# Optimization experiments

Hardware: AMD Instinct MI355X
Metric: run time of the kernel (lower is better)

## Reference

```python
import jax, jax.numpy as jnp
import numpy as np

B, S, HID = 1, 2048, 4096
H, KV, D, R = 32, 8, 128, 64   # heads, kv heads, head_dim, rotary_dim
EPS = 1e-6
THETA = 10000.0


def setup_inputs() -> dict:
    key = jax.random.key(0)
    ks = jax.random.split(key, 6)
    sc = 0.02
    return {
        'hidden_states': jax.random.normal(ks[0], (B, S, HID), jnp.float32),
        'Wq': jax.random.normal(ks[1], (H * D, HID), jnp.float32) * sc,
        'Wk': jax.random.normal(ks[2], (KV * D, HID), jnp.float32) * sc,
        'Wv': jax.random.normal(ks[3], (KV * D, HID), jnp.float32) * sc,
        'Wo': jax.random.normal(ks[4], (HID, H * D), jnp.float32) * sc,
        'q_norm_w': jnp.ones((H * D,), jnp.float32),
        'k_norm_w': jnp.ones((KV * D,), jnp.float32),
        'position_ids': jnp.broadcast_to(jnp.arange(S, dtype=jnp.int64)[None, :], (B, S)),
    }


def _rms_norm(x, w):
    xf = x.astype(jnp.float32)
    var = jnp.mean(xf * xf, axis=-1, keepdims=True)
    return (w * (xf * jax.lax.rsqrt(var + EPS))).astype(x.dtype)


def _rotate_half(x):
    x1, x2 = x[..., : R // 2], x[..., R // 2:]
    return jnp.concatenate((-x2, x1), axis=-1)


def reference(hidden_states, Wq, Wk, Wv, Wo, q_norm_w, k_norm_w, position_ids):
    x = hidden_states
    # projections (torch Linear: y = x @ W^T)
    q = jnp.einsum('bsd,od->bso', x, Wq)                      # [B,S,H*D]
    k = jnp.einsum('bsd,od->bso', x, Wk)                      # [B,S,KV*D]
    v = jnp.einsum('bsd,od->bso', x, Wv).reshape(B, S, KV, D)
    # QK RMSNorm over flattened head dims
    q = _rms_norm(q, q_norm_w).reshape(B, S, H, D)
    k = _rms_norm(k, k_norm_w).reshape(B, S, KV, D)
    # partial RoPE: rotary_dim=R out of head_dim=D
    inv_freq = 1.0 / (THETA ** (jnp.arange(0, R, 2, dtype=jnp.float32) / R))  # [R/2]
    freqs = position_ids.astype(jnp.float32)[..., None] * inv_freq            # [B,S,R/2]
    emb = jnp.concatenate((freqs, freqs), axis=-1)                            # [B,S,R]
    cos = jnp.cos(emb)[:, :, None, :]                                         # [B,S,1,R]
    sin = jnp.sin(emb)[:, :, None, :]
    q_rot = q[..., :R] * cos + _rotate_half(q[..., :R]) * sin
    k_rot = k[..., :R] * cos + _rotate_half(k[..., :R]) * sin
    q = jnp.concatenate((q_rot, q[..., R:]), axis=-1)
    k = jnp.concatenate((k_rot, k[..., R:]), axis=-1)
    # GQA repeat_kv
    G = H // KV
    k = jnp.repeat(k, G, axis=2)  # [B,S,H,D]
    v = jnp.repeat(v, G, axis=2)
    # attention with causal mask, softmax in fp32
    scaling = D ** -0.5
    scores = jnp.einsum('bqhd,bkhd->bhqk', q, k) * scaling    # [B,H,S,S]
    causal = jnp.tril(jnp.ones((S, S), dtype=bool))
    scores = jnp.where(causal[None, None], scores, jnp.finfo(jnp.float32).min)
    attn = jax.nn.softmax(scores.astype(jnp.float32), axis=-1).astype(q.dtype)
    out = jnp.einsum('bhqk,bkhd->bqhd', attn, v).reshape(B, S, H * D)
    return jnp.einsum('bso,do->bsd', out, Wo)
```

## Files before the change

kernel.cpp:

```cpp
#include <hip/hip_runtime.h>
#include <hip/hip_bf16.h>
#include <math.h>

typedef __bf16 bf16;
typedef __bf16 bf16x8 __attribute__((ext_vector_type(8)));
typedef float f32x4 __attribute__((ext_vector_type(4)));

#define S_LEN 2048
#define HID_D 4096
#define NH 32
#define NKV 8
#define HD 128
#define SCALE_LOG2 (0.08838834764831843f * 1.4426950408889634f)
#define FIXED_M 17.0f

__device__ __forceinline__ void gload_lds16(const void* g, void* lds) {
  __builtin_amdgcn_global_load_lds((__attribute__((address_space(1))) void*)g,
                                   (__attribute__((address_space(3))) void*)lds, 16, 0, 0);
}

#define MEMFENCE asm volatile("" ::: "memory")

__device__ __forceinline__ void cvt_range(const float* __restrict__ in,
                                          bf16* __restrict__ out, int n8,
                                          int start, int stride) {
  for (int i = start; i < n8; i += stride) {
    const float4* p = (const float4*)in + 2 * (size_t)i;
    float4 a = p[0], b = p[1];
    bf16x8 o;
    o[0] = (bf16)a.x; o[1] = (bf16)a.y; o[2] = (bf16)a.z; o[3] = (bf16)a.w;
    o[4] = (bf16)b.x; o[5] = (bf16)b.y; o[6] = (bf16)b.z; o[7] = (bf16)b.w;
    *((bf16x8*)out + i) = o;
  }
}

__global__ __launch_bounds__(256) void cvt4_kernel(const float* __restrict__ s0,
                                                   const float* __restrict__ s1,
                                                   const float* __restrict__ s2,
                                                   const float* __restrict__ s3,
                                                   bf16* __restrict__ d0,
                                                   bf16* __restrict__ d1,
                                                   bf16* __restrict__ d2,
                                                   bf16* __restrict__ d3,
                                                   int n0, int n1, int n2, int n3) {
  int start = blockIdx.x * blockDim.x + threadIdx.x;
  int stride = gridDim.x * blockDim.x;
  cvt_range(s0, d0, n0, start, stride);
  cvt_range(s1, d1, n1, start, stride);
  cvt_range(s2, d2, n2, start, stride);
  cvt_range(s3, d3, n3, start, stride);
}

__global__ __launch_bounds__(256) void cvt_kernel(const float* __restrict__ in,
                                                  bf16* __restrict__ out, int n8) {
  int i = blockIdx.x * blockDim.x + threadIdx.x;
  int stride = gridDim.x * blockDim.x;
  cvt_range(in, out, n8, i, stride);
}

template <int BM, int BN>
__global__ __launch_bounds__(512, 2) void gemm_s(const bf16* __restrict__ A,
                                                 const bf16* __restrict__ B,
                                                 float* __restrict__ C,
                                                 int N, int Kfull, int T) {
  constexpr int MFr = BM / 32;
  constexpr int NFr = BN / 64;
  constexpr int NL = (BM + BN) / 64;
  constexpr int TILE = (BM + BN) * 128;

  __shared__ __align__(16) char lds[2 * TILE];
  const int t = threadIdx.x, l = t & 63, w = t >> 6;
  const int wr = w >> 2, wc = w & 3;
  const int l15 = l & 15, lg = l >> 4;

  const int GX = gridDim.x, GY = gridDim.y;
  const int lin = blockIdx.y * GX + blockIdx.x;
  const int x = lin & 7, j = lin >> 3;
  const int rectW = GX >> 2, rectH = GY >> 1;
  const int rx = x & 3, ry = x >> 2;
  const int jn = j % rectW, jm = j / rectW;
  const int n0 = (rx * rectW + jn) * BN;
  const int m0 = (ry * rectH + jm) * BM;

  auto stage = [&](int d, int tau) {
    char* dst = lds + d * TILE;
    const size_t kpos = (size_t)tau * 64;
#pragma unroll
    for (int i = 0; i < NL; i++) {
      int q = i * 512 + t;
      int r = q >> 3;
      int c = (q & 7) ^ (r & 7);
      const bf16* src = (i * 512 < BM * 8)
                            ? (A + (size_t)(m0 + r) * Kfull)
                            : (B + (size_t)(n0 + (r - BM)) * Kfull);
      gload_lds16(src + kpos + c * 8, dst + q * 16);
    }
  };

  f32x4 acc[MFr][NFr] = {};

  stage(0, 0);
  asm volatile("s_waitcnt vmcnt(0)" ::: "memory");
  MEMFENCE; __builtin_amdgcn_s_barrier(); MEMFENCE;

  for (int tau = 0; tau < T; tau++) {
    const int d = tau & 1;
    if (tau + 1 < T) stage(d ^ 1, tau + 1);

    const char* Ab = lds + d * TILE;
    const char* Bb = Ab + BM * 128;
    bf16x8 a[MFr][2], b[NFr][2];
#pragma unroll
    for (int mf = 0; mf < MFr; mf++) {
      const int row = wr * (BM / 2) + mf * 16 + l15;
#pragma unroll
      for (int ks = 0; ks < 2; ks++)
        a[mf][ks] = *(const bf16x8*)(Ab + row * 128 + (((ks * 4 + lg) ^ (row & 7)) << 4));
    }
#pragma unroll
    for (int nf = 0; nf < NFr; nf++) {
      const int row = wc * (BN / 4) + nf * 16 + l15;
#pragma unroll
      for (int ks = 0; ks < 2; ks++)
        b[nf][ks] = *(const bf16x8*)(Bb + row * 128 + (((ks * 4 + lg) ^ (row & 7)) << 4));
    }
#pragma unroll
    for (int mf = 0; mf < MFr; mf++)
#pragma unroll
      for (int nf = 0; nf < NFr; nf++)
#pragma unroll
        for (int ks = 0; ks < 2; ks++)
          acc[mf][nf] = __builtin_amdgcn_mfma_f32_16x16x32_bf16(a[mf][ks], b[nf][ks],
                                                               acc[mf][nf], 0, 0, 0);

    asm volatile("s_waitcnt vmcnt(0)" ::: "memory");
    MEMFENCE; __builtin_amdgcn_s_barrier(); MEMFENCE;
  }

#pragma unroll
  for (int mf = 0; mf < MFr; mf++) {
    int row = m0 + wr * (BM / 2) + mf * 16 + lg * 4;
#pragma unroll
    for (int nf = 0; nf < NFr; nf++) {
      int col = n0 + wc * (BN / 4) + nf * 16 + l15;
      float* Cp = C + (size_t)row * N + col;
#pragma unroll
      for (int rr = 0; rr < 4; rr++) Cp[(size_t)rr * N] = acc[mf][nf][rr];
    }
  }
}

__global__ __launch_bounds__(256) void vt_kernel(const float* __restrict__ QKV,
                                                 bf16* __restrict__ Vt) {
  __shared__ __align__(16) float tile[64][68];
  const int s0 = blockIdx.x * 64, d0 = blockIdx.y * 64;
  const int t = threadIdx.x;
#pragma unroll
  for (int i = 0; i < 4; i++) {
    int row = i * 16 + (t >> 4);
    int c4 = t & 15;
    float4 v = *(const float4*)(QKV + (size_t)(s0 + row) * 6144 + 5120 + d0 + c4 * 4);
    *(float4*)&tile[row][c4 * 4] = v;
  }
  __syncthreads();
#pragma unroll
  for (int i = 0; i < 2; i++) {
    int slot = i * 256 + t;
    int dr = slot >> 3, ch = slot & 7;
    bf16x8 o;
#pragma unroll
    for (int j = 0; j < 8; j++) o[j] = (bf16)tile[ch * 8 + j][dr];
    *(bf16x8*)(Vt + (size_t)(d0 + dr) * S_LEN + s0 + ch * 8) = o;
  }
}

__global__ __launch_bounds__(256) void prep_kernel(const float* __restrict__ QKV,
                                                   const float* __restrict__ qw,
                                                   const float* __restrict__ kw,
                                                   const int* __restrict__ pos_ids,
                                                   bf16* __restrict__ Qb,
                                                   bf16* __restrict__ Kb) {
  __shared__ __align__(16) float row[5120];
  __shared__ float cs[64];
  __shared__ float red[8];
  const int s = blockIdx.x, t = threadIdx.x;

  const float4* src = (const float4*)(QKV + (size_t)s * 6144);
#pragma unroll
  for (int i = 0; i < 5; i++) ((float4*)row)[t + i * 256] = src[t + i * 256];

  if (t < 32) {
    float p = (float)pos_ids[s];
    float ang = p * powf(10000.0f, -(float)t * (1.0f / 32.0f));
    float sn, cn;
    sincosf(ang, &sn, &cn);
    cs[t] = cn;
    cs[32 + t] = sn;
  }
  __syncthreads();

  float aq = 0.f, ak = 0.f;
  for (int i = t; i < 4096; i += 256) { float v = row[i]; aq += v * v; }
  for (int i = 4096 + t; i < 5120; i += 256) { float v = row[i]; ak += v * v; }
#pragma unroll
  for (int off = 32; off; off >>= 1) {
    aq += __shfl_down(aq, off);
    ak += __shfl_down(ak, off);
  }
  if ((t & 63) == 0) { red[t >> 6] = aq; red[4 + (t >> 6)] = ak; }
  __syncthreads();
  const float scq = rsqrtf((red[0] + red[1] + red[2] + red[3]) * (1.0f / 4096.0f) + 1e-6f);
  const float sck = rsqrtf((red[4] + red[5] + red[6] + red[7]) * (1.0f / 1024.0f) + 1e-6f);

  for (int e = t; e < 4096; e += 256) {
    int d = e & 127;
    int hh = e >> 7;
    float val = row[e] * scq * qw[e];
    float o;
    if (d < 32)       o = val * cs[d] - (row[e + 32] * scq * qw[e + 32]) * cs[32 + d];
    else if (d < 64)  o = val * cs[d - 32] + (row[e - 32] * scq * qw[e - 32]) * cs[d];
    else              o = val;
    Qb[((size_t)hh * S_LEN + s) * HD + d] = (bf16)o;
  }
  for (int e = t; e < 1024; e += 256) {
    int d = e & 127;
    int hh = e >> 7;
    int ri = 4096 + e;
    float val = row[ri] * sck * kw[e];
    float o;
    if (d < 32)       o = val * cs[d] - (row[ri + 32] * sck * kw[e + 32]) * cs[32 + d];
    else if (d < 64)  o = val * cs[d - 32] + (row[ri - 32] * sck * kw[e - 32]) * cs[d];
    else              o = val;
    Kb[((size_t)hh * S_LEN + s) * HD + d] = (bf16)o;
  }
}

__global__ __launch_bounds__(256, 2) void attn_kernel(const bf16* __restrict__ Qb,
                                                      const bf16* __restrict__ Kb,
                                                      const bf16* __restrict__ Vt,
                                                      bf16* __restrict__ Ctx) {
  __shared__ __align__(16) char KB[2][16384];
  __shared__ __align__(16) char VB[2][16384];
  __shared__ __align__(16) char PB[8192];
  const int t = threadIdx.x, l = t & 63, w = t >> 6;
  const int l15 = l & 15, lg = l >> 4;
  const int pairc = blockIdx.x >> 5;
  const int h = blockIdx.x & 31;

  const bf16* Kh = Kb + (size_t)(h >> 2) * S_LEN * HD;
  const bf16* Vh = Vt + (size_t)(h >> 2) * HD * S_LEN;
  char* Pw = PB + w * 2048;

  const int kj0 = t & 15;
  const int vj0 = t & 7;

  auto stageK = [&](int buf, int kvbase) {
#pragma unroll
    for (int i = 0; i < 4; i++) {
      int r = (i * 256 + t) >> 4;
      const bf16* src = Kh + (size_t)(kvbase + r) * HD + ((kj0 ^ (r & 7)) << 3);
      gload_lds16(src, KB[buf] + (i * 256 + w * 64) * 16);
    }
  };
  auto stageV = [&](int buf, int kvbase) {
#pragma unroll
    for (int i = 0; i < 4; i++) {
      int r = (i * 256 + t) >> 3;
      const bf16* src = Vh + (size_t)r * S_LEN + kvbase + ((vj0 ^ (r & 7)) << 3);
      gload_lds16(src, VB[buf] + (i * 256 + w * 64) * 16);
    }
  };

#pragma unroll
  for (int phase = 0; phase < 2; phase++) {
    const int chunk = (phase == 0) ? pairc : (31 - pairc);
    const int ktiles = chunk + 1;
    const int q0 = chunk * 64 + w * 16;

    const bf16* Qh = Qb + ((size_t)h * S_LEN + q0) * HD;
    bf16x8 qf[4];
#pragma unroll
    for (int kk = 0; kk < 4; kk++)
      qf[kk] = *(const bf16x8*)(Qh + (size_t)l15 * HD + kk * 32 + lg * 8);

    stageK(0, 0);
    stageV(0, 0);

    f32x4 O[8] = {};
    float lsum[4] = {0.f, 0.f, 0.f, 0.f};

    for (int tt = 0; tt < ktiles; tt++) {
      const int cur = tt & 1;
      const int kv0 = tt * 64;
      const char* Kcur = KB[cur];
      const bool hasnext = (tt + 1 < ktiles);

      asm volatile("s_waitcnt vmcnt(0)" ::: "memory");
      MEMFENCE;
      __builtin_amdgcn_s_barrier();
      MEMFENCE;

      if (hasnext) {
        stageK(cur ^ 1, kv0 + 64);
        stageV(cur ^ 1, kv0 + 64);
      }

      f32x4 sc[4];
#pragma unroll
      for (int g = 0; g < 4; g++) sc[g] = (f32x4){0.f, 0.f, 0.f, 0.f};
#pragma unroll
      for (int g = 0; g < 4; g++) {
        const int r = g * 16 + l15;
        const char* Krow = Kcur + r * 256;
        const int sw = (r & 7);
#pragma unroll
        for (int kk = 0; kk < 4; kk++) {
          bf16x8 kf = *(const bf16x8*)(Krow + (((kk * 4 + lg) ^ sw) << 4));
          sc[g] = __builtin_amdgcn_mfma_f32_16x16x32_bf16(qf[kk], kf, sc[g], 0, 0, 0);
        }
      }

      const bool needmask = (kv0 + 63 > q0);
      float sv[4][4];
#pragma unroll
      for (int g = 0; g < 4; g++)
#pragma unroll
        for (int r = 0; r < 4; r++) {
          float x = fmaf(sc[g][r], SCALE_LOG2, -FIXED_M);
          if (needmask) {
            int kv = kv0 + g * 16 + l15;
            int qr = q0 + lg * 4 + r;
            if (kv > qr) x = -1e30f;
          }
          sv[g][r] = exp2f(x);
        }
#pragma unroll
      for (int r = 0; r < 4; r++)
        lsum[r] += (sv[0][r] + sv[1][r]) + (sv[2][r] + sv[3][r]);

#pragma unroll
      for (int g = 0; g < 4; g++)
#pragma unroll
        for (int r = 0; r < 4; r++) {
          int prow = lg * 4 + r;
          int csw = (prow & 3) ^ (((prow >> 2) & 3) << 1);
          int pbyte = prow * 128 + (((g * 16 + l15) * 2) ^ (csw << 4));
          *(bf16*)(Pw + pbyte) = (bf16)sv[g][r];
        }
      asm volatile("s_waitcnt lgkmcnt(0)" ::: "memory");
      const int rcsw = (l15 & 3) ^ (((l15 >> 2) & 3) << 1);
      bf16x8 pa[2];
#pragma unroll
      for (int ks = 0; ks < 2; ks++)
        pa[ks] = *(const bf16x8*)(Pw + l15 * 128 + (((ks * 4 + lg) ^ rcsw) << 4));

#pragma unroll
      for (int ks = 0; ks < 2; ks++)
#pragma unroll
        for (int dt = 0; dt < 8; dt++) {
          const int r = dt * 16 + l15;
          bf16x8 vf = *(const bf16x8*)(VB[cur] + r * 128 + (((ks * 4 + lg) ^ (r & 7)) << 4));
          O[dt] = __builtin_amdgcn_mfma_f32_16x16x32_bf16(pa[ks], vf, O[dt], 0, 0, 0);
        }
    }

    MEMFENCE;
    __builtin_amdgcn_s_barrier();
    MEMFENCE;

#pragma unroll
    for (int r = 0; r < 4; r++) {
      float x = lsum[r];
      x += __shfl_xor(x, 1);
      x += __shfl_xor(x, 2);
      x += __shfl_xor(x, 4);
      x += __shfl_xor(x, 8);
      float inv = 1.0f / x;
      bf16* Cp = Ctx + (size_t)(q0 + lg * 4 + r) * HID_D + h * HD + l15;
#pragma unroll
      for (int dt = 0; dt < 8; dt++) Cp[dt * 16] = (bf16)(O[dt][r] * inv);
    }
  }
}

extern "C" void kernel_launch(void* const* d_in, const int* in_sizes, int n_in,
                              void* d_out, int out_size, void* d_ws, size_t ws_size,
                              hipStream_t stream) {
  const float* X  = (const float*)d_in[0];
  const float* Wq = (const float*)d_in[1];
  const float* Wk = (const float*)d_in[2];
  const float* Wv = (const float*)d_in[3];
  const float* Wo = (const float*)d_in[4];
  const float* qw = (const float*)d_in[5];
  const float* kw = (const float*)d_in[6];
  const int* pos  = (const int*)d_in[7];

  char* ws = (char*)d_ws;
  bf16* Xb    = (bf16*)ws;
  bf16* Wqkvb = (bf16*)(ws + (16ll << 20));
  bf16* Wob   = Wqkvb;
  float* QKV  = (float*)(ws + (64ll << 20));
  bf16* Ctx   = (bf16*)(ws + (96ll << 20));
  bf16* Qb    = (bf16*)(ws + (112ll << 20));
  bf16* Kb    = (bf16*)(ws + (128ll << 20));
  bf16* Vt    = (bf16*)(ws + (132ll << 20));

  cvt4_kernel<<<2048, 256, 0, stream>>>(X, Wq, Wk, Wv,
                                        Xb, Wqkvb, Wqkvb + 4096 * 4096,
                                        Wqkvb + 5120 * 4096,
                                        S_LEN * HID_D / 8, 4096 * 4096 / 8,
                                        1024 * 4096 / 8, 1024 * 4096 / 8);

  gemm_s<128, 384><<<dim3(16, 16), 512, 0, stream>>>(Xb, Wqkvb, QKV, 6144, HID_D, 64);

  cvt_kernel<<<2048, 256, 0, stream>>>(Wo, Wob, 4096 * 4096 / 8);

  vt_kernel<<<dim3(32, 16), 256, 0, stream>>>(QKV, Vt);
  prep_kernel<<<S_LEN, 256, 0, stream>>>(QKV, qw, kw, pos, Qb, Kb);

  attn_kernel<<<dim3(512), 256, 0, stream>>>(Qb, Kb, Vt, Ctx);

  gemm_s<128, 256><<<dim3(16, 16), 512, 0, stream>>>(Ctx, Wob, (float*)d_out,
                                                     HID_D, HID_D, 64);
}
```

Baseline: 318.6 us.

## Deepen GEMM pipeline to four 32-wide K stages and delay attention prefetch

The GEMM is restructured from a double-buffered loop with 64-wide K steps into a four-buffer loop with 32-wide K steps. It keeps three loads in flight, waits on partial vmcnt counts instead of draining them, and uses a swizzle adjusted to the 64-byte rows. The goal is to hide global-load latency behind the MFMAs. The cost is twice as many barriers per K, fewer MFMAs per barrier, and hand-set vmcnt counts that depend on NL. In the attention kernel, the next K/V tile prefetch now issues after the QK^T MFMAs, which shifts when memory traffic overlaps compute.

```diff
diff --git a/kernel.cpp b/kernel.cpp
--- a/kernel.cpp
+++ b/kernel.cpp
@@ -59,16 +59,16 @@
 }
 
 template <int BM, int BN>
-__global__ __launch_bounds__(512, 2) void gemm_s(const bf16* __restrict__ A,
+__global__ __launch_bounds__(512, 2) void gemm_p(const bf16* __restrict__ A,
                                                  const bf16* __restrict__ B,
                                                  float* __restrict__ C,
                                                  int N, int Kfull, int T) {
   constexpr int MFr = BM / 32;
   constexpr int NFr = BN / 64;
-  constexpr int NL = (BM + BN) / 64;
-  constexpr int TILE = (BM + BN) * 128;
-
-  __shared__ __align__(16) char lds[2 * TILE];
+  constexpr int NL = (BM + BN) / 128;
+  constexpr int TILE = (BM + BN) * 64;
+
+  __shared__ __align__(16) char lds[4 * TILE];
   const int t = threadIdx.x, l = t & 63, w = t >> 6;
   const int wr = w >> 2, wc = w & 3;
   const int l15 = l & 15, lg = l >> 4;
@@ -82,58 +82,61 @@
   const int n0 = (rx * rectW + jn) * BN;
   const int m0 = (ry * rectH + jm) * BM;
 
-  auto stage = [&](int d, int tau) {
-    char* dst = lds + d * TILE;
-    const size_t kpos = (size_t)tau * 64;
+  auto stage = [&](int buf, int tau) {
+    char* dst = lds + buf * TILE;
+    const size_t kpos = (size_t)tau * 32;
 #pragma unroll
     for (int i = 0; i < NL; i++) {
       int q = i * 512 + t;
-      int r = q >> 3;
-      int c = (q & 7) ^ (r & 7);
-      const bf16* src = (i * 512 < BM * 8)
-                            ? (A + (size_t)(m0 + r) * Kfull)
-                            : (B + (size_t)(n0 + (r - BM)) * Kfull);
+      int r = q >> 2;
+      int c = (q & 3) ^ ((r >> 1) & 3);
+      const bf16* src = (r < BM) ? (A + (size_t)(m0 + r) * Kfull)
+                                 : (B + (size_t)(n0 + (r - BM)) * Kfull);
       gload_lds16(src + kpos + c * 8, dst + q * 16);
     }
   };
 
   f32x4 acc[MFr][NFr] = {};
 
-  stage(0, 0);
-  asm volatile("s_waitcnt vmcnt(0)" ::: "memory");
+  stage(0, 0); stage(1, 1); stage(2, 2);
+  if (NL == 4) { asm volatile("s_waitcnt vmcnt(8)" ::: "memory"); }
+  else         { asm volatile("s_waitcnt vmcnt(6)" ::: "memory"); }
   MEMFENCE; __builtin_amdgcn_s_barrier(); MEMFENCE;
 
   for (int tau = 0; tau < T; tau++) {
-    const int d = tau & 1;
-    if (tau + 1 < T) stage(d ^ 1, tau + 1);
+    const int d = tau & 3;
+    if (tau + 3 < T) stage((tau + 3) & 3, tau + 3);
 
     const char* Ab = lds + d * TILE;
-    const char* Bb = Ab + BM * 128;
-    bf16x8 a[MFr][2], b[NFr][2];
+    const char* Bb = Ab + BM * 64;
+    bf16x8 a[MFr], b[NFr];
 #pragma unroll
     for (int mf = 0; mf < MFr; mf++) {
       const int row = wr * (BM / 2) + mf * 16 + l15;
-#pragma unroll
-      for (int ks = 0; ks < 2; ks++)
-        a[mf][ks] = *(const bf16x8*)(Ab + row * 128 + (((ks * 4 + lg) ^ (row & 7)) << 4));
+      a[mf] = *(const bf16x8*)(Ab + row * 64 + ((lg ^ ((row >> 1) & 3)) << 4));
     }
 #pragma unroll
     for (int nf = 0; nf < NFr; nf++) {
       const int row = wc * (BN / 4) + nf * 16 + l15;
-#pragma unroll
-      for (int ks = 0; ks < 2; ks++)
-        b[nf][ks] = *(const bf16x8*)(Bb + row * 128 + (((ks * 4 + lg) ^ (row & 7)) << 4));
+      b[nf] = *(const bf16x8*)(Bb + row * 64 + ((lg ^ ((row >> 1) & 3)) << 4));
     }
 #pragma unroll
     for (int mf = 0; mf < MFr; mf++)
 #pragma unroll
       for (int nf = 0; nf < NFr; nf++)
-#pragma unroll
-        for (int ks = 0; ks < 2; ks++)
-          acc[mf][nf] = __builtin_amdgcn_mfma_f32_16x16x32_bf16(a[mf][ks], b[nf][ks],
-                                                               acc[mf][nf], 0, 0, 0);
-
-    asm volatile("s_waitcnt vmcnt(0)" ::: "memory");
+        acc[mf][nf] = __builtin_amdgcn_mfma_f32_16x16x32_bf16(a[mf], b[nf],
+                                                             acc[mf][nf], 0, 0, 0);
+
+    const int k = T - 2 - tau;
+    if (NL == 4) {
+      if (k >= 2)      { asm volatile("s_waitcnt vmcnt(8)" ::: "memory"); }
+      else if (k == 1) { asm volatile("s_waitcnt vmcnt(4)" ::: "memory"); }
+      else             { asm volatile("s_waitcnt vmcnt(0)" ::: "memory"); }
+    } else {
+      if (k >= 2)      { asm volatile("s_waitcnt vmcnt(6)" ::: "memory"); }
+      else if (k == 1) { asm volatile("s_waitcnt vmcnt(3)" ::: "memory"); }
+      else             { asm volatile("s_waitcnt vmcnt(0)" ::: "memory"); }
+    }
     MEMFENCE; __builtin_amdgcn_s_barrier(); MEMFENCE;
   }
 
@@ -300,11 +303,6 @@
       __builtin_amdgcn_s_barrier();
       MEMFENCE;
 
-      if (hasnext) {
-        stageK(cur ^ 1, kv0 + 64);
-        stageV(cur ^ 1, kv0 + 64);
-      }
-
       f32x4 sc[4];
 #pragma unroll
       for (int g = 0; g < 4; g++) sc[g] = (f32x4){0.f, 0.f, 0.f, 0.f};
@@ -318,6 +316,11 @@
           bf16x8 kf = *(const bf16x8*)(Krow + (((kk * 4 + lg) ^ sw) << 4));
           sc[g] = __builtin_amdgcn_mfma_f32_16x16x32_bf16(qf[kk], kf, sc[g], 0, 0, 0);
         }
+      }
+
+      if (hasnext) {
+        stageK(cur ^ 1, kv0 + 64);
+        stageV(cur ^ 1, kv0 + 64);
       }
 
       const bool needmask = (kv0 + 63 > q0);
@@ -411,7 +414,7 @@
                                         S_LEN * HID_D / 8, 4096 * 4096 / 8,
                                         1024 * 4096 / 8, 1024 * 4096 / 8);
 
-  gemm_s<128, 384><<<dim3(16, 16), 512, 0, stream>>>(Xb, Wqkvb, QKV, 6144, HID_D, 64);
+  gemm_p<128, 384><<<dim3(16, 16), 512, 0, stream>>>(Xb, Wqkvb, QKV, 6144, HID_D, 128);
 
   cvt_kernel<<<2048, 256, 0, stream>>>(Wo, Wob, 4096 * 4096 / 8);
 
@@ -420,6 +423,6 @@
 
   attn_kernel<<<dim3(512), 256, 0, stream>>>(Qb, Kb, Vt, Ctx);
 
-  gemm_s<128, 256><<<dim3(16, 16), 512, 0, stream>>>(Ctx, Wob, (float*)d_out,
-                                                     HID_D, HID_D, 64);
-}
+  gemm_p<128, 256><<<dim3(16, 16), 512, 0, stream>>>(Ctx, Wob, (float*)d_out,
+                                                     HID_D, HID_D, 128);
+}
```

After: 333.5 us. +4.7%, slower.

## Split-K output projection with larger tiles and move attention KV prefetch after QK

Applied to the files above, without the earlier changes.

Replaces the output-projection GEMM with a split-K variant that uses 256x256 tiles over two K halves. The halves are written to the output and to a workspace partial buffer, then summed by a separate add kernel. This keeps the grid at 256 blocks while raising per-block data reuse, at the cost of an extra 32MB read-modify-write pass and a slightly different accumulation order. Separately, the attention kernel now issues the next K/V tile loads after the QK MFMAs rather than before them, which changes how those loads overlap with compute.

```diff
diff --git a/kernel.cpp b/kernel.cpp
--- a/kernel.cpp
+++ b/kernel.cpp
@@ -58,6 +58,18 @@
   cvt_range(in, out, n8, i, stride);
 }
 
+__global__ __launch_bounds__(256) void add_kernel(float* __restrict__ out,
+                                                  const float* __restrict__ part, int n4) {
+  int i = blockIdx.x * blockDim.x + threadIdx.x;
+  int stride = gridDim.x * blockDim.x;
+  for (; i < n4; i += stride) {
+    float4 a = ((const float4*)out)[i];
+    float4 b = ((const float4*)part)[i];
+    a.x += b.x; a.y += b.y; a.z += b.z; a.w += b.w;
+    ((float4*)out)[i] = a;
+  }
+}
+
 template <int BM, int BN>
 __global__ __launch_bounds__(512, 2) void gemm_s(const bf16* __restrict__ A,
                                                  const bf16* __restrict__ B,
@@ -132,6 +144,98 @@
         for (int ks = 0; ks < 2; ks++)
           acc[mf][nf] = __builtin_amdgcn_mfma_f32_16x16x32_bf16(a[mf][ks], b[nf][ks],
                                                                acc[mf][nf], 0, 0, 0);
+
+    asm volatile("s_waitcnt vmcnt(0)" ::: "memory");
+    MEMFENCE; __builtin_amdgcn_s_barrier(); MEMFENCE;
+  }
+
+#pragma unroll
+  for (int mf = 0; mf < MFr; mf++) {
+    int row = m0 + wr * (BM / 2) + mf * 16 + lg * 4;
+#pragma unroll
+    for (int nf = 0; nf < NFr; nf++) {
+      int col = n0 + wc * (BN / 4) + nf * 16 + l15;
+      float* Cp = C + (size_t)row * N + col;
+#pragma unroll
+      for (int rr = 0; rr < 4; rr++) Cp[(size_t)rr * N] = acc[mf][nf][rr];
+    }
+  }
+}
+
+template <int BM, int BN>
+__global__ __launch_bounds__(512, 2) void gemm_sk(const bf16* __restrict__ A,
+                                                  const bf16* __restrict__ B,
+                                                  float* __restrict__ C0,
+                                                  float* __restrict__ C1,
+                                                  int N, int Kfull, int Kslice, int T) {
+  constexpr int MFr = BM / 32;
+  constexpr int NFr = BN / 64;
+  constexpr int NL = (BM + BN) / 64;
+  constexpr int TILE = (BM + BN) * 128;
+
+  __shared__ __align__(16) char lds[2 * TILE];
+  const int t = threadIdx.x, l = t & 63, w = t >> 6;
+  const int wr = w >> 2, wc = w & 3;
+  const int l15 = l & 15, lg = l >> 4;
+
+  const int GX = gridDim.x, GY = gridDim.y;
+  const int lin = blockIdx.y * GX + blockIdx.x;
+  const int x = lin & 7, j = lin >> 3;
+  const int rectW = GX >> 2, rectH = GY >> 1;
+  const int rx = x & 3, ry = x >> 2;
+  const int jn = j % rectW, jm = j / rectW;
+  const int n0 = (rx * rectW + jn) * BN;
+  const int m0 = (ry * rectH + jm) * BM;
+  const size_t kbase = (size_t)blockIdx.z * Kslice;
+  float* __restrict__ C = blockIdx.z ? C1 : C0;
+
+  auto stage = [&](int d, int tau) {
+    char* dst = lds + d * TILE;
+    const size_t kpos = kbase + (size_t)tau * 64;
+#pragma unroll
+    for (int i = 0; i < NL; i++) {
+      int q = i * 512 + t;
+      int r = q >> 3;
+      int c = (q & 7) ^ (r & 7);
+      const bf16* src = (i * 512 < BM * 8)
+                            ? (A + (size_t)(m0 + r) * Kfull)
+                            : (B + (size_t)(n0 + (r - BM)) * Kfull);
+      gload_lds16(src + kpos + c * 8, dst + q * 16);
+    }
+  };
+
+  f32x4 acc[MFr][NFr] = {};
+
+  stage(0, 0);
+  asm volatile("s_waitcnt vmcnt(0)" ::: "memory");
+  MEMFENCE; __builtin_amdgcn_s_barrier(); MEMFENCE;
+
+  for (int tau = 0; tau < T; tau++) {
+    const int d = tau & 1;
+    if (tau + 1 < T) stage(d ^ 1, tau + 1);
+
+    const char* Ab = lds + d * TILE;
+    const char* Bb = Ab + BM * 128;
+#pragma unroll
+    for (int ks = 0; ks < 2; ks++) {
+      bf16x8 a[MFr], b[NFr];
+#pragma unroll
+      for (int mf = 0; mf < MFr; mf++) {
+        const int row = wr * (BM / 2) + mf * 16 + l15;
+        a[mf] = *(const bf16x8*)(Ab + row * 128 + (((ks * 4 + lg) ^ (row & 7)) << 4));
+      }
+#pragma unroll
+      for (int nf = 0; nf < NFr; nf++) {
+        const int row = wc * (BN / 4) + nf * 16 + l15;
+        b[nf] = *(const bf16x8*)(Bb + row * 128 + (((ks * 4 + lg) ^ (row & 7)) << 4));
+      }
+#pragma unroll
+      for (int mf = 0; mf < MFr; mf++)
+#pragma unroll
+        for (int nf = 0; nf < NFr; nf++)
+          acc[mf][nf] = __builtin_amdgcn_mfma_f32_16x16x32_bf16(a[mf], b[nf],
+                                                               acc[mf][nf], 0, 0, 0);
+    }
 
     asm volatile("s_waitcnt vmcnt(0)" ::: "memory");
     MEMFENCE; __builtin_amdgcn_s_barrier(); MEMFENCE;
@@ -300,11 +404,6 @@
       __builtin_amdgcn_s_barrier();
       MEMFENCE;
 
-      if (hasnext) {
-        stageK(cur ^ 1, kv0 + 64);
-        stageV(cur ^ 1, kv0 + 64);
-      }
-
       f32x4 sc[4];
 #pragma unroll
       for (int g = 0; g < 4; g++) sc[g] = (f32x4){0.f, 0.f, 0.f, 0.f};
@@ -318,6 +417,11 @@
           bf16x8 kf = *(const bf16x8*)(Krow + (((kk * 4 + lg) ^ sw) << 4));
           sc[g] = __builtin_amdgcn_mfma_f32_16x16x32_bf16(qf[kk], kf, sc[g], 0, 0, 0);
         }
+      }
+
+      if (hasnext) {
+        stageK(cur ^ 1, kv0 + 64);
+        stageV(cur ^ 1, kv0 + 64);
       }
 
       const bool needmask = (kv0 + 63 > q0);
@@ -400,6 +504,7 @@
   bf16* Wqkvb = (bf16*)(ws + (16ll << 20));
   bf16* Wob   = Wqkvb;
   float* QKV  = (float*)(ws + (64ll << 20));
+  float* Part = (float*)(ws + (64ll << 20));
   bf16* Ctx   = (bf16*)(ws + (96ll << 20));
   bf16* Qb    = (bf16*)(ws + (112ll << 20));
   bf16* Kb    = (bf16*)(ws + (128ll << 20));
@@ -420,6 +525,7 @@
 
   attn_kernel<<<dim3(512), 256, 0, stream>>>(Qb, Kb, Vt, Ctx);
 
-  gemm_s<128, 256><<<dim3(16, 16), 512, 0, stream>>>(Ctx, Wob, (float*)d_out,
-                                                     HID_D, HID_D, 64);
-}
+  gemm_sk<256, 256><<<dim3(16, 8, 2), 512, 0, stream>>>(Ctx, Wob, (float*)d_out, Part,
+                                                        HID_D, HID_D, 2048, 32);
+  add_kernel<<<2048, 256, 0, stream>>>((float*)d_out, Part, S_LEN * HID_D / 4);
+}
```

Measured after the change: 323.8 us. Within noise of the previous version (+1.6%).
